# Kernel optimization log

Measured on AMD Instinct MI355X. Metric: run time of the kernel, lower is better.

## Reference

```python
import jax, jax.numpy as jnp
import numpy as np

NUM_EXPERTS = 8
TOP_K = 2
HIDDEN = 1024
INTER = 3584
B, S = 1, 2048


def setup_inputs() -> dict:
    key = jax.random.key(0)
    k0, k1, k2, k3, k4 = jax.random.split(key, 5)
    scale = 0.02
    return {
        "hidden_states": jax.random.normal(k0, (B, S, HIDDEN), dtype=jnp.float32),
        "gate_w": jax.random.normal(k1, (NUM_EXPERTS, HIDDEN), dtype=jnp.float32) * scale,
        "w1": jax.random.normal(k2, (NUM_EXPERTS, INTER, HIDDEN), dtype=jnp.float32) * scale,
        "w2": jax.random.normal(k3, (NUM_EXPERTS, HIDDEN, INTER), dtype=jnp.float32) * scale,
        "w3": jax.random.normal(k4, (NUM_EXPERTS, INTER, HIDDEN), dtype=jnp.float32) * scale,
    }


def reference(hidden_states, gate_w, w1, w2, w3):
    b, s, h = hidden_states.shape
    x = hidden_states.reshape(-1, h)  # [T, H]
    T = x.shape[0]

    # Router: softmax in float32, take top-k, renormalize (normalize_routing_weights=1)
    router_logits = x @ gate_w.T  # [T, E]
    routing_probs = jax.nn.softmax(router_logits.astype(jnp.float32), axis=-1)
    top_w, top_i = jax.lax.top_k(routing_probs, TOP_K)  # [T, K]
    top_w = top_w / jnp.sum(top_w, axis=-1, keepdims=True)
    top_w = top_w.astype(x.dtype)

    # Dense per-token gate matrix [T, E]: weight if expert selected, else 0.
    rows = jnp.arange(T)[:, None]
    gates = jnp.zeros((T, NUM_EXPERTS), dtype=x.dtype).at[rows, top_i].set(top_w)

    # Equivalent to gather-MLP-scatter: y = sum_e gate[:,e] * SwiGLU_e(x)
    out = jnp.zeros((T, h), dtype=x.dtype)
    for e in range(NUM_EXPERTS):
        hid = jax.nn.silu(x @ w1[e].T) * (x @ w3[e].T)  # [T, F]
        out = out + (hid @ w2[e].T) * gates[:, e:e + 1]
    return out.reshape(b, s, h)
```

## Files before the change

### kernel.cpp

```cpp
#include <hip/hip_runtime.h>
#include <hip/hip_bf16.h>
#include <stdint.h>

#define T_TOKENS 2048
#define HID_DIM 1024
#define INTER 3584
#define NEXP 8
#define PTILES 40

typedef float f32x4 __attribute__((ext_vector_type(4)));
typedef short short8 __attribute__((ext_vector_type(8)));
typedef unsigned short ushort8 __attribute__((ext_vector_type(8)));

#define AS1 __attribute__((address_space(1)))
#define AS3 __attribute__((address_space(3)))

__device__ __forceinline__ void gload_lds16(const void* g, void* l) {
    __builtin_amdgcn_global_load_lds((AS1 void*)g, (AS3 void*)l, 16, 0, 0);
}

__device__ __forceinline__ f32x4 mfma16(short8 a, short8 b, f32x4 c) {
    return __builtin_amdgcn_mfma_f32_16x16x32_bf16(a, b, c, 0, 0, 0);
}

__device__ __forceinline__ unsigned short f2bf(float f) {
    union { __hip_bfloat16 h; unsigned short u; } cv;
    cv.h = __float2bfloat16(f);
    return cv.u;
}

__device__ __forceinline__ ushort8 cvt8(float4 v0, float4 v1) {
    ushort8 u;
    u[0] = f2bf(v0.x); u[1] = f2bf(v0.y); u[2] = f2bf(v0.z); u[3] = f2bf(v0.w);
    u[4] = f2bf(v1.x); u[5] = f2bf(v1.y); u[6] = f2bf(v1.z); u[7] = f2bf(v1.w);
    return u;
}

__global__ __launch_bounds__(256) void pack_w_k(const float* __restrict__ w1, const float* __restrict__ w2,
                                                const float* __restrict__ w3,
                                                unsigned short* __restrict__ w1p,
                                                unsigned short* __restrict__ w3p,
                                                unsigned short* __restrict__ w2p) {
    int which = blockIdx.z;
    int e = blockIdx.y;
    const float* src;
    unsigned short* dst;
    int NT, KT, K;
    if (which == 0) { src = w1; dst = w1p; NT = 56; KT = 16; K = HID_DIM; }
    else if (which == 1) { src = w3; dst = w3p; NT = 56; KT = 16; K = HID_DIM; }
    else { src = w2; dst = w2p; NT = 16; KT = 56; K = INTER; }
    int nt = blockIdx.x % NT;
    int kt = blockIdx.x / NT;

    int col = threadIdx.x & 63;
    int kq = threadIdx.x >> 6;
    const float* s = src + ((size_t)(e * (NT * 64) + nt * 64 + col)) * K + kt * 64 + kq * 16;
    float4 v0 = *reinterpret_cast<const float4*>(s);
    float4 v1 = *reinterpret_cast<const float4*>(s + 4);
    float4 v2 = *reinterpret_cast<const float4*>(s + 8);
    float4 v3 = *reinterpret_cast<const float4*>(s + 12);
    unsigned short* d = dst + ((size_t)(e * NT + nt) * KT + kt) * 4096;
    *reinterpret_cast<ushort8*>(d + ((kq * 2 + 0) * 64 + col) * 8) = cvt8(v0, v1);
    *reinterpret_cast<ushort8*>(d + ((kq * 2 + 1) * 64 + col) * 8) = cvt8(v2, v3);
}

__global__ void router_k(const float* __restrict__ x, const float* __restrict__ gw,
                         int* __restrict__ topk_e, float* __restrict__ topk_w,
                         int* __restrict__ ctl) {
    int lane = threadIdx.x & 63;
    int wid = threadIdx.x >> 6;
    int t = blockIdx.x * 4 + wid;
    const float* xr = x + (size_t)t * HID_DIM;

    float acc[NEXP];
#pragma unroll
    for (int e = 0; e < NEXP; ++e) acc[e] = 0.f;

#pragma unroll
    for (int j = 0; j < 4; ++j) {
        int c = j * 256 + lane * 4;
        float4 v = *reinterpret_cast<const float4*>(xr + c);
#pragma unroll
        for (int e = 0; e < NEXP; ++e) {
            float4 g = *reinterpret_cast<const float4*>(gw + e * HID_DIM + c);
            acc[e] += v.x * g.x + v.y * g.y + v.z * g.z + v.w * g.w;
        }
    }
#pragma unroll
    for (int off = 32; off > 0; off >>= 1)
#pragma unroll
        for (int e = 0; e < NEXP; ++e) acc[e] += __shfl_xor(acc[e], off, 64);

    if (lane == 0) {
        int e0 = 0;
#pragma unroll
        for (int e = 1; e < NEXP; ++e) if (acc[e] > acc[e0]) e0 = e;
        int e1 = -1;
        float b1 = 0.f;
#pragma unroll
        for (int e = 0; e < NEXP; ++e) {
            if (e == e0) continue;
            if (e1 < 0 || acc[e] > b1) { e1 = e; b1 = acc[e]; }
        }
        float p1 = __expf(b1 - acc[e0]);
        float s = 1.f + p1;
        topk_e[2 * t] = e0; topk_e[2 * t + 1] = e1;
        topk_w[2 * t] = 1.f / s; topk_w[2 * t + 1] = p1 / s;
        atomicAdd(&ctl[e0], 1);
        atomicAdd(&ctl[e1], 1);
    }
}

__global__ void prefix_k(int* __restrict__ ctl) {
    if (threadIdx.x == 0) {
        int r = 0;
        for (int e = 0; e < NEXP; ++e) {
            ctl[32 + e] = r;
            r += (ctl[e] + 127) & ~127;
            ctl[16 + e] = 0;
        }
    }
}

__global__ void scatter_k(const int* __restrict__ topk_e, const float* __restrict__ topk_w,
                          int* __restrict__ ctl, int* __restrict__ perm_token,
                          float* __restrict__ perm_gate) {
    int t = blockIdx.x * 256 + threadIdx.x;
    if (t >= T_TOKENS) return;
#pragma unroll
    for (int k = 0; k < 2; ++k) {
        int e = topk_e[2 * t + k];
        int p = ctl[32 + e] + atomicAdd(&ctl[16 + e], 1);
        perm_token[p] = t;
        perm_gate[p] = topk_w[2 * t + k];
    }
}

__global__ __launch_bounds__(256) void pack_x_k(const float* __restrict__ x,
                                                const int* __restrict__ perm_token,
                                                unsigned short* __restrict__ xgp) {
    int ptile = blockIdx.x;
    int kt = blockIdx.y;
    int row = threadIdx.x & 127;
    int kh = threadIdx.x >> 7;
    int tok = perm_token[ptile * 128 + row];
    const float* s = x + (size_t)tok * HID_DIM + kt * 64 + kh * 32;
    unsigned short* d = xgp + (size_t)ptile * 131072 + (size_t)kt * 8192;
#pragma unroll
    for (int kb2 = 0; kb2 < 4; ++kb2) {
        int kb = kh * 4 + kb2;
        float4 v0 = *reinterpret_cast<const float4*>(s + kb2 * 8);
        float4 v1 = *reinterpret_cast<const float4*>(s + kb2 * 8 + 4);
        *reinterpret_cast<ushort8*>(d + (kb * 128 + row) * 8) = cvt8(v0, v1);
    }
}

__global__ __launch_bounds__(256) void gemm1_k(
    const unsigned short* __restrict__ xgp,
    const unsigned short* __restrict__ w1p, const unsigned short* __restrict__ w3p,
    const int* __restrict__ ctl, unsigned short* __restrict__ hidp) {
    int e = blockIdx.z;
    int cnt = ctl[e];
    int tm = blockIdx.x;
    if (tm * 128 >= cnt) return;
    int off = ctl[32 + e];
    int nt = blockIdx.y;
    int ptile = (off >> 7) + tm;

    __shared__ __attribute__((aligned(16))) unsigned short A_l[8192];
    __shared__ __attribute__((aligned(16))) unsigned short B1_l[4096];
    __shared__ __attribute__((aligned(16))) unsigned short B3_l[4096];

    int tid = threadIdx.x;
    int lane = tid & 63;
    int wid = tid >> 6;
    int wr = wid >> 1, wc = wid & 1;
    int q = lane >> 4, rr = lane & 15;

    const unsigned short* asrc = xgp + (size_t)ptile * 131072;
    const unsigned short* b1s = w1p + (size_t)(e * 56 + nt) * 65536;
    const unsigned short* b3s = w3p + (size_t)(e * 56 + nt) * 65536;

    f32x4 acc1[4][2], acc3[4][2];
#pragma unroll
    for (int i = 0; i < 4; ++i)
#pragma unroll
        for (int j = 0; j < 2; ++j) { acc1[i][j] = 0.f; acc3[i][j] = 0.f; }

    for (int kt = 0; kt < 16; ++kt) {
        const unsigned short* as = asrc + (size_t)kt * 8192;
        const unsigned short* b1 = b1s + (size_t)kt * 4096;
        const unsigned short* b3 = b3s + (size_t)kt * 4096;
#pragma unroll
        for (int c = 0; c < 4; ++c)
            gload_lds16(as + (c * 256 + tid) * 8, A_l + (c * 256 + tid) * 8);
#pragma unroll
        for (int c = 0; c < 2; ++c) {
            gload_lds16(b1 + (c * 256 + tid) * 8, B1_l + (c * 256 + tid) * 8);
            gload_lds16(b3 + (c * 256 + tid) * 8, B3_l + (c * 256 + tid) * 8);
        }
        __syncthreads();
#pragma unroll
        for (int kk = 0; kk < 2; ++kk) {
            short8 a[4], b1v[2], b3v[2];
            const unsigned short* abase = A_l + (size_t)((kk * 4 + q) * 128 + wr * 64 + rr) * 8;
#pragma unroll
            for (int i = 0; i < 4; ++i) a[i] = *reinterpret_cast<const short8*>(abase + i * 16 * 8);
            const unsigned short* b1base = B1_l + (size_t)((kk * 4 + q) * 64 + wc * 32 + rr) * 8;
            const unsigned short* b3base = B3_l + (size_t)((kk * 4 + q) * 64 + wc * 32 + rr) * 8;
#pragma unroll
            for (int j = 0; j < 2; ++j) {
                b1v[j] = *reinterpret_cast<const short8*>(b1base + j * 16 * 8);
                b3v[j] = *reinterpret_cast<const short8*>(b3base + j * 16 * 8);
            }
#pragma unroll
            for (int i = 0; i < 4; ++i)
#pragma unroll
                for (int j = 0; j < 2; ++j) {
                    acc1[i][j] = mfma16(a[i], b1v[j], acc1[i][j]);
                    acc3[i][j] = mfma16(a[i], b3v[j], acc3[i][j]);
                }
        }
        __syncthreads();
    }

    int rbase = wr * 64 + q * 4;
    int colb = wc * 32 + rr;
    unsigned short* hb = hidp + (size_t)(ptile * 56 + nt) * 8192;
#pragma unroll
    for (int i = 0; i < 4; ++i) {
#pragma unroll
        for (int r = 0; r < 4; ++r) {
            int lrow = rbase + i * 16 + r;
            if (tm * 128 + lrow < cnt) {
#pragma unroll
                for (int j = 0; j < 2; ++j) {
                    int col = colb + j * 16;
                    float g = acc1[i][j][r];
                    float u = acc3[i][j][r];
                    float h = (g / (1.f + __expf(-g))) * u;
                    hb[((col >> 3) * 128 + lrow) * 8 + (col & 7)] = f2bf(h);
                }
            }
        }
    }
}

__global__ __launch_bounds__(256) void gemm2_k(
    const unsigned short* __restrict__ hidp, const unsigned short* __restrict__ w2p,
    const int* __restrict__ ctl, const int* __restrict__ perm_token,
    const float* __restrict__ perm_gate, float* __restrict__ out) {
    int e = blockIdx.z;
    int cnt = ctl[e];
    int tm = blockIdx.x;
    if (tm * 128 >= cnt) return;
    int off = ctl[32 + e];
    int ptile = (off >> 7) + tm;

    __shared__ __attribute__((aligned(16))) unsigned short A_l[8192];
    __shared__ __attribute__((aligned(16))) unsigned short B_l[8192];

    int tid = threadIdx.x;
    int lane = tid & 63;
    int wid = tid >> 6;
    int wr = wid >> 1, wc = wid & 1;
    int q = lane >> 4, rr = lane & 15;

    const unsigned short* asrc = hidp + (size_t)(ptile * 56) * 8192;
    const unsigned short* bs0 = w2p + (size_t)(e * 16 + 2 * blockIdx.y) * 229376;
    const unsigned short* bs1 = bs0 + 229376;

    f32x4 acc[4][4];
#pragma unroll
    for (int i = 0; i < 4; ++i)
#pragma unroll
        for (int j = 0; j < 4; ++j) acc[i][j] = 0.f;

    for (int kt = 0; kt < 56; ++kt) {
        const unsigned short* as = asrc + (size_t)kt * 8192;
        const unsigned short* b0 = bs0 + (size_t)kt * 4096;
        const unsigned short* b1 = bs1 + (size_t)kt * 4096;
#pragma unroll
        for (int c = 0; c < 4; ++c)
            gload_lds16(as + (c * 256 + tid) * 8, A_l + (c * 256 + tid) * 8);
#pragma unroll
        for (int c = 0; c < 2; ++c) {
            gload_lds16(b0 + (c * 256 + tid) * 8, B_l + (c * 256 + tid) * 8);
            gload_lds16(b1 + (c * 256 + tid) * 8, B_l + 4096 + (c * 256 + tid) * 8);
        }
        __syncthreads();
#pragma unroll
        for (int kk = 0; kk < 2; ++kk) {
            short8 a[4], b[4];
            const unsigned short* abase = A_l + (size_t)((kk * 4 + q) * 128 + wr * 64 + rr) * 8;
            const unsigned short* bbase = B_l + (size_t)(wc * 4096) + (size_t)((kk * 4 + q) * 64 + rr) * 8;
#pragma unroll
            for (int i = 0; i < 4; ++i) a[i] = *reinterpret_cast<const short8*>(abase + i * 16 * 8);
#pragma unroll
            for (int j = 0; j < 4; ++j) b[j] = *reinterpret_cast<const short8*>(bbase + j * 16 * 8);
#pragma unroll
            for (int i = 0; i < 4; ++i)
#pragma unroll
                for (int j = 0; j < 4; ++j) acc[i][j] = mfma16(a[i], b[j], acc[i][j]);
        }
        __syncthreads();
    }

    int rb = wr * 64 + q * 4;
    int hb = blockIdx.y * 128 + wc * 64 + rr;
#pragma unroll
    for (int i = 0; i < 4; ++i) {
#pragma unroll
        for (int r = 0; r < 4; ++r) {
            int lrow = rb + i * 16 + r;
            int grow = tm * 128 + lrow;
            if (grow < cnt) {
                int p = off + grow;
                int tok = perm_token[p];
                float gate = perm_gate[p];
#pragma unroll
                for (int j = 0; j < 4; ++j)
                    atomicAdd(&out[(size_t)tok * HID_DIM + hb + j * 16], acc[i][j][r] * gate);
            }
        }
    }
}

extern "C" void kernel_launch(void* const* d_in, const int* in_sizes, int n_in,
                              void* d_out, int out_size, void* d_ws, size_t ws_size,
                              hipStream_t stream) {
    const float* x  = (const float*)d_in[0];
    const float* gw = (const float*)d_in[1];
    const float* w1 = (const float*)d_in[2];
    const float* w2 = (const float*)d_in[3];
    const float* w3 = (const float*)d_in[4];
    float* out = (float*)d_out;

    char* ws = (char*)d_ws;
    int*   ctl        = (int*)ws;
    int*   topk_e     = (int*)(ws + 4096);
    float* topk_w     = (float*)(ws + 20480);
    int*   perm_token = (int*)(ws + 36864);
    float* perm_gate  = (float*)(ws + 57344);
    unsigned short* xgp  = (unsigned short*)(ws + (1ull << 20));
    unsigned short* hidp = (unsigned short*)(ws + 12582912);
    unsigned short* w1p  = (unsigned short*)(ws + 52428800);
    unsigned short* w3p  = (unsigned short*)(ws + 111149056);
    unsigned short* w2p  = (unsigned short*)(ws + 169869312);

    hipMemsetAsync(ctl, 0, 256, stream);
    hipMemsetAsync(perm_token, 0, PTILES * 128 * sizeof(int), stream);
    hipMemsetAsync(out, 0, (size_t)out_size * sizeof(float), stream);

    pack_w_k<<<dim3(896, NEXP, 3), 256, 0, stream>>>(w1, w2, w3, w1p, w3p, w2p);
    router_k<<<dim3(T_TOKENS / 4), 256, 0, stream>>>(x, gw, topk_e, topk_w, ctl);
    prefix_k<<<dim3(1), 64, 0, stream>>>(ctl);
    scatter_k<<<dim3(T_TOKENS / 256), 256, 0, stream>>>(topk_e, topk_w, ctl, perm_token, perm_gate);
    pack_x_k<<<dim3(PTILES, 16), 256, 0, stream>>>(x, perm_token, xgp);
    gemm1_k<<<dim3(PTILES, INTER / 64, NEXP), 256, 0, stream>>>(xgp, w1p, w3p, ctl, hidp);
    gemm2_k<<<dim3(PTILES, HID_DIM / 128, NEXP), 256, 0, stream>>>(hidp, w2p, ctl, perm_token, perm_gate, out);
}
```

Measured before the change: 421.8 us.

## Drop weight pre-pack; stream fp32 weights once per expert tile in GEMMs

Removes the separate pack_w_k pass that converted all expert weights to bf16 in a workspace, which cost a full read of the fp32 weights plus a bf16 write and re-read. The GEMM kernels now load fp32 weight slices directly, convert them to bf16 in LDS with register prefetch of the next k-step, and loop over all token tiles of an expert inside one block so each weight slice is read once. gemm2 also splits K in two with atomics. A operands are read straight from global without LDS staging, which may raise load latency and cost bandwidth.

New measurement: 459.6 us. 9.0% more time.

```diff
diff --git a/kernel.cpp b/kernel.cpp
--- a/kernel.cpp
+++ b/kernel.cpp
@@ -12,13 +12,6 @@
 typedef short short8 __attribute__((ext_vector_type(8)));
 typedef unsigned short ushort8 __attribute__((ext_vector_type(8)));
 
-#define AS1 __attribute__((address_space(1)))
-#define AS3 __attribute__((address_space(3)))
-
-__device__ __forceinline__ void gload_lds16(const void* g, void* l) {
-    __builtin_amdgcn_global_load_lds((AS1 void*)g, (AS3 void*)l, 16, 0, 0);
-}
-
 __device__ __forceinline__ f32x4 mfma16(short8 a, short8 b, f32x4 c) {
     return __builtin_amdgcn_mfma_f32_16x16x32_bf16(a, b, c, 0, 0, 0);
 }
@@ -36,32 +29,10 @@
     return u;
 }
 
-__global__ __launch_bounds__(256) void pack_w_k(const float* __restrict__ w1, const float* __restrict__ w2,
-                                                const float* __restrict__ w3,
-                                                unsigned short* __restrict__ w1p,
-                                                unsigned short* __restrict__ w3p,
-                                                unsigned short* __restrict__ w2p) {
-    int which = blockIdx.z;
-    int e = blockIdx.y;
-    const float* src;
-    unsigned short* dst;
-    int NT, KT, K;
-    if (which == 0) { src = w1; dst = w1p; NT = 56; KT = 16; K = HID_DIM; }
-    else if (which == 1) { src = w3; dst = w3p; NT = 56; KT = 16; K = HID_DIM; }
-    else { src = w2; dst = w2p; NT = 16; KT = 56; K = INTER; }
-    int nt = blockIdx.x % NT;
-    int kt = blockIdx.x / NT;
-
-    int col = threadIdx.x & 63;
-    int kq = threadIdx.x >> 6;
-    const float* s = src + ((size_t)(e * (NT * 64) + nt * 64 + col)) * K + kt * 64 + kq * 16;
-    float4 v0 = *reinterpret_cast<const float4*>(s);
-    float4 v1 = *reinterpret_cast<const float4*>(s + 4);
-    float4 v2 = *reinterpret_cast<const float4*>(s + 8);
-    float4 v3 = *reinterpret_cast<const float4*>(s + 12);
-    unsigned short* d = dst + ((size_t)(e * NT + nt) * KT + kt) * 4096;
-    *reinterpret_cast<ushort8*>(d + ((kq * 2 + 0) * 64 + col) * 8) = cvt8(v0, v1);
-    *reinterpret_cast<ushort8*>(d + ((kq * 2 + 1) * 64 + col) * 8) = cvt8(v2, v3);
+__device__ __forceinline__ ushort4 cvt4(float4 v) {
+    ushort4 u;
+    u.x = f2bf(v.x); u.y = f2bf(v.y); u.z = f2bf(v.z); u.w = f2bf(v.w);
+    return u;
 }
 
 __global__ void router_k(const float* __restrict__ x, const float* __restrict__ gw,
@@ -155,172 +126,187 @@
     }
 }
 
-__global__ __launch_bounds__(256) void gemm1_k(
+__global__ __launch_bounds__(512) void gemm1_k(
     const unsigned short* __restrict__ xgp,
-    const unsigned short* __restrict__ w1p, const unsigned short* __restrict__ w3p,
+    const float* __restrict__ w1, const float* __restrict__ w3,
     const int* __restrict__ ctl, unsigned short* __restrict__ hidp) {
-    int e = blockIdx.z;
+    int e = blockIdx.x & 7;
+    int nt = blockIdx.x >> 3;
     int cnt = ctl[e];
-    int tm = blockIdx.x;
-    if (tm * 128 >= cnt) return;
-    int off = ctl[32 + e];
-    int nt = blockIdx.y;
-    int ptile = (off >> 7) + tm;
-
-    __shared__ __attribute__((aligned(16))) unsigned short A_l[8192];
-    __shared__ __attribute__((aligned(16))) unsigned short B1_l[4096];
-    __shared__ __attribute__((aligned(16))) unsigned short B3_l[4096];
+    if (cnt == 0) return;
+    int ntm = (cnt + 127) >> 7;
+    int pt0 = ctl[32 + e] >> 7;
+
+    __shared__ __attribute__((aligned(16))) unsigned short B_l[8 * 66 * 8];
 
     int tid = threadIdx.x;
     int lane = tid & 63;
-    int wid = tid >> 6;
-    int wr = wid >> 1, wc = wid & 1;
+    int w = tid >> 6;
     int q = lane >> 4, rr = lane & 15;
 
-    const unsigned short* asrc = xgp + (size_t)ptile * 131072;
-    const unsigned short* b1s = w1p + (size_t)(e * 56 + nt) * 65536;
-    const unsigned short* b3s = w3p + (size_t)(e * 56 + nt) * 65536;
-
-    f32x4 acc1[4][2], acc3[4][2];
-#pragma unroll
-    for (int i = 0; i < 4; ++i)
-#pragma unroll
-        for (int j = 0; j < 2; ++j) { acc1[i][j] = 0.f; acc3[i][j] = 0.f; }
-
-    for (int kt = 0; kt < 16; ++kt) {
-        const unsigned short* as = asrc + (size_t)kt * 8192;
-        const unsigned short* b1 = b1s + (size_t)kt * 4096;
-        const unsigned short* b3 = b3s + (size_t)kt * 4096;
-#pragma unroll
-        for (int c = 0; c < 4; ++c)
-            gload_lds16(as + (c * 256 + tid) * 8, A_l + (c * 256 + tid) * 8);
-#pragma unroll
-        for (int c = 0; c < 2; ++c) {
-            gload_lds16(b1 + (c * 256 + tid) * 8, B1_l + (c * 256 + tid) * 8);
-            gload_lds16(b3 + (c * 256 + tid) * 8, B3_l + (c * 256 + tid) * 8);
-        }
-        __syncthreads();
-#pragma unroll
-        for (int kk = 0; kk < 2; ++kk) {
-            short8 a[4], b1v[2], b3v[2];
-            const unsigned short* abase = A_l + (size_t)((kk * 4 + q) * 128 + wr * 64 + rr) * 8;
-#pragma unroll
-            for (int i = 0; i < 4; ++i) a[i] = *reinterpret_cast<const short8*>(abase + i * 16 * 8);
-            const unsigned short* b1base = B1_l + (size_t)((kk * 4 + q) * 64 + wc * 32 + rr) * 8;
-            const unsigned short* b3base = B3_l + (size_t)((kk * 4 + q) * 64 + wc * 32 + rr) * 8;
-#pragma unroll
-            for (int j = 0; j < 2; ++j) {
-                b1v[j] = *reinterpret_cast<const short8*>(b1base + j * 16 * 8);
-                b3v[j] = *reinterpret_cast<const short8*>(b3base + j * 16 * 8);
-            }
-#pragma unroll
-            for (int i = 0; i < 4; ++i)
+    int brow = tid >> 3;
+    int ko = (tid & 7) * 8;
+    const float* wsrc = (brow & 32) ? w3 : w1;
+    const float* bsrc = wsrc + ((size_t)e * INTER + nt * 32 + (brow & 31)) * HID_DIM + ko;
+    int bo = ((tid & 7) * 66 + brow) * 8;
+
+    for (int base = 0; base < ntm; base += 4) {
+        const unsigned short* at[4];
+#pragma unroll
+        for (int tt = 0; tt < 4; ++tt) {
+            int idx = base + tt;
+            at[tt] = xgp + (size_t)(pt0 + (idx < ntm ? idx : 0)) * 131072;
+        }
+        f32x4 acc1[4][2], acc3[4][2];
+#pragma unroll
+        for (int tt = 0; tt < 4; ++tt)
+#pragma unroll
+            for (int j = 0; j < 2; ++j) { acc1[tt][j] = 0.f; acc3[tt][j] = 0.f; }
+
+        float4 f0 = *reinterpret_cast<const float4*>(bsrc);
+        float4 f1 = *reinterpret_cast<const float4*>(bsrc + 4);
+        for (int kt = 0; kt < 16; ++kt) {
+            *reinterpret_cast<ushort8*>(B_l + bo) = cvt8(f0, f1);
+            __syncthreads();
+            if (kt < 15) {
+                f0 = *reinterpret_cast<const float4*>(bsrc + (kt + 1) * 64);
+                f1 = *reinterpret_cast<const float4*>(bsrc + (kt + 1) * 64 + 4);
+            }
+#pragma unroll
+            for (int kk = 0; kk < 2; ++kk) {
+                int ar = ((kk * 4 + q) * 128 + w * 16 + rr) * 8;
+                short8 a[4];
+#pragma unroll
+                for (int tt = 0; tt < 4; ++tt)
+                    a[tt] = *reinterpret_cast<const short8*>(at[tt] + (size_t)kt * 8192 + ar);
+                const unsigned short* bb = B_l + ((kk * 4 + q) * 66 + rr) * 8;
+                short8 b1v[2], b3v[2];
+                b1v[0] = *reinterpret_cast<const short8*>(bb);
+                b1v[1] = *reinterpret_cast<const short8*>(bb + 128);
+                b3v[0] = *reinterpret_cast<const short8*>(bb + 256);
+                b3v[1] = *reinterpret_cast<const short8*>(bb + 384);
+#pragma unroll
+                for (int tt = 0; tt < 4; ++tt)
+#pragma unroll
+                    for (int j = 0; j < 2; ++j) {
+                        acc1[tt][j] = mfma16(a[tt], b1v[j], acc1[tt][j]);
+                        acc3[tt][j] = mfma16(a[tt], b3v[j], acc3[tt][j]);
+                    }
+            }
+            __syncthreads();
+        }
+
+        int lrow = w * 16 + q * 4;
+        int tile56 = nt >> 1;
+        int colbase = (nt & 1) * 32;
+#pragma unroll
+        for (int tt = 0; tt < 4; ++tt) {
+            if (base + tt < ntm) {
+                size_t hb = (size_t)((pt0 + base + tt) * 56 + tile56) * 8192;
+                int rowoff = (base + tt) * 128 + lrow;
 #pragma unroll
                 for (int j = 0; j < 2; ++j) {
-                    acc1[i][j] = mfma16(a[i], b1v[j], acc1[i][j]);
-                    acc3[i][j] = mfma16(a[i], b3v[j], acc3[i][j]);
+                    int hcol = colbase + j * 16 + rr;
+                    int kb = hcol >> 3, w8 = hcol & 7;
+#pragma unroll
+                    for (int ri = 0; ri < 4; ++ri) {
+                        if (rowoff + ri < cnt) {
+                            float g = acc1[tt][j][ri];
+                            float u = acc3[tt][j][ri];
+                            float h = (g / (1.f + __expf(-g))) * u;
+                            hidp[hb + (kb * 128 + lrow + ri) * 8 + w8] = f2bf(h);
+                        }
+                    }
                 }
-        }
-        __syncthreads();
-    }
-
-    int rbase = wr * 64 + q * 4;
-    int colb = wc * 32 + rr;
-    unsigned short* hb = hidp + (size_t)(ptile * 56 + nt) * 8192;
-#pragma unroll
-    for (int i = 0; i < 4; ++i) {
-#pragma unroll
-        for (int r = 0; r < 4; ++r) {
-            int lrow = rbase + i * 16 + r;
-            if (tm * 128 + lrow < cnt) {
-#pragma unroll
-                for (int j = 0; j < 2; ++j) {
-                    int col = colb + j * 16;
-                    float g = acc1[i][j][r];
-                    float u = acc3[i][j][r];
-                    float h = (g / (1.f + __expf(-g))) * u;
-                    hb[((col >> 3) * 128 + lrow) * 8 + (col & 7)] = f2bf(h);
-                }
-            }
-        }
-    }
-}
-
-__global__ __launch_bounds__(256) void gemm2_k(
-    const unsigned short* __restrict__ hidp, const unsigned short* __restrict__ w2p,
+            }
+        }
+    }
+}
+
+__global__ __launch_bounds__(512) void gemm2_k(
+    const unsigned short* __restrict__ hidp, const float* __restrict__ w2,
     const int* __restrict__ ctl, const int* __restrict__ perm_token,
     const float* __restrict__ perm_gate, float* __restrict__ out) {
-    int e = blockIdx.z;
+    int e = blockIdx.x & 7;
+    int nt = (blockIdx.x >> 3) & 31;
+    int ks = blockIdx.x >> 8;
     int cnt = ctl[e];
-    int tm = blockIdx.x;
-    if (tm * 128 >= cnt) return;
+    if (cnt == 0) return;
+    int ntm = (cnt + 127) >> 7;
     int off = ctl[32 + e];
-    int ptile = (off >> 7) + tm;
-
-    __shared__ __attribute__((aligned(16))) unsigned short A_l[8192];
-    __shared__ __attribute__((aligned(16))) unsigned short B_l[8192];
+    int pt0 = off >> 7;
+
+    __shared__ __attribute__((aligned(16))) unsigned short B_l[8 * 34 * 8];
 
     int tid = threadIdx.x;
     int lane = tid & 63;
-    int wid = tid >> 6;
-    int wr = wid >> 1, wc = wid & 1;
+    int w = tid >> 6;
     int q = lane >> 4, rr = lane & 15;
 
-    const unsigned short* asrc = hidp + (size_t)(ptile * 56) * 8192;
-    const unsigned short* bs0 = w2p + (size_t)(e * 16 + 2 * blockIdx.y) * 229376;
-    const unsigned short* bs1 = bs0 + 229376;
-
-    f32x4 acc[4][4];
-#pragma unroll
-    for (int i = 0; i < 4; ++i)
-#pragma unroll
-        for (int j = 0; j < 4; ++j) acc[i][j] = 0.f;
-
-    for (int kt = 0; kt < 56; ++kt) {
-        const unsigned short* as = asrc + (size_t)kt * 8192;
-        const unsigned short* b0 = bs0 + (size_t)kt * 4096;
-        const unsigned short* b1 = bs1 + (size_t)kt * 4096;
-#pragma unroll
-        for (int c = 0; c < 4; ++c)
-            gload_lds16(as + (c * 256 + tid) * 8, A_l + (c * 256 + tid) * 8);
-#pragma unroll
-        for (int c = 0; c < 2; ++c) {
-            gload_lds16(b0 + (c * 256 + tid) * 8, B_l + (c * 256 + tid) * 8);
-            gload_lds16(b1 + (c * 256 + tid) * 8, B_l + 4096 + (c * 256 + tid) * 8);
-        }
-        __syncthreads();
-#pragma unroll
-        for (int kk = 0; kk < 2; ++kk) {
-            short8 a[4], b[4];
-            const unsigned short* abase = A_l + (size_t)((kk * 4 + q) * 128 + wr * 64 + rr) * 8;
-            const unsigned short* bbase = B_l + (size_t)(wc * 4096) + (size_t)((kk * 4 + q) * 64 + rr) * 8;
-#pragma unroll
-            for (int i = 0; i < 4; ++i) a[i] = *reinterpret_cast<const short8*>(abase + i * 16 * 8);
-#pragma unroll
-            for (int j = 0; j < 4; ++j) b[j] = *reinterpret_cast<const short8*>(bbase + j * 16 * 8);
-#pragma unroll
-            for (int i = 0; i < 4; ++i)
-#pragma unroll
-                for (int j = 0; j < 4; ++j) acc[i][j] = mfma16(a[i], b[j], acc[i][j]);
-        }
-        __syncthreads();
-    }
-
-    int rb = wr * 64 + q * 4;
-    int hb = blockIdx.y * 128 + wc * 64 + rr;
-#pragma unroll
-    for (int i = 0; i < 4; ++i) {
-#pragma unroll
-        for (int r = 0; r < 4; ++r) {
-            int lrow = rb + i * 16 + r;
-            int grow = tm * 128 + lrow;
-            if (grow < cnt) {
-                int p = off + grow;
-                int tok = perm_token[p];
-                float gate = perm_gate[p];
-#pragma unroll
-                for (int j = 0; j < 4; ++j)
-                    atomicAdd(&out[(size_t)tok * HID_DIM + hb + j * 16], acc[i][j][r] * gate);
+    int brow = tid >> 4;
+    int ko = (tid & 15) * 4;
+    const float* bsrc = w2 + ((size_t)e * HID_DIM + nt * 32 + brow) * INTER + (size_t)ks * 28 * 64 + ko;
+    int bo = ((ko >> 3) * 34 + brow) * 8 + (ko & 7);
+
+    int kt0 = ks * 28;
+    for (int base = 0; base < ntm; base += 4) {
+        const unsigned short* at[4];
+#pragma unroll
+        for (int tt = 0; tt < 4; ++tt) {
+            int idx = base + tt;
+            at[tt] = hidp + (size_t)(pt0 + (idx < ntm ? idx : 0)) * 56 * 8192;
+        }
+        f32x4 acc[4][2];
+#pragma unroll
+        for (int tt = 0; tt < 4; ++tt)
+#pragma unroll
+            for (int j = 0; j < 2; ++j) acc[tt][j] = 0.f;
+
+        float4 f0 = *reinterpret_cast<const float4*>(bsrc);
+        for (int t = 0; t < 28; ++t) {
+            int kt = kt0 + t;
+            *reinterpret_cast<ushort4*>(B_l + bo) = cvt4(f0);
+            __syncthreads();
+            if (t < 27) f0 = *reinterpret_cast<const float4*>(bsrc + (t + 1) * 64);
+#pragma unroll
+            for (int kk = 0; kk < 2; ++kk) {
+                int ar = ((kk * 4 + q) * 128 + w * 16 + rr) * 8;
+                short8 a[4];
+#pragma unroll
+                for (int tt = 0; tt < 4; ++tt)
+                    a[tt] = *reinterpret_cast<const short8*>(at[tt] + (size_t)kt * 8192 + ar);
+                const unsigned short* bb = B_l + ((kk * 4 + q) * 34 + rr) * 8;
+                short8 b[2];
+                b[0] = *reinterpret_cast<const short8*>(bb);
+                b[1] = *reinterpret_cast<const short8*>(bb + 128);
+#pragma unroll
+                for (int tt = 0; tt < 4; ++tt)
+#pragma unroll
+                    for (int j = 0; j < 2; ++j)
+                        acc[tt][j] = mfma16(a[tt], b[j], acc[tt][j]);
+            }
+            __syncthreads();
+        }
+
+        int lrow = w * 16 + q * 4;
+#pragma unroll
+        for (int tt = 0; tt < 4; ++tt) {
+            if (base + tt < ntm) {
+                int rowoff = (base + tt) * 128 + lrow;
+#pragma unroll
+                for (int ri = 0; ri < 4; ++ri) {
+                    int grow = rowoff + ri;
+                    if (grow < cnt) {
+                        int p = off + grow;
+                        int tok = perm_token[p];
+                        float gate = perm_gate[p];
+#pragma unroll
+                        for (int j = 0; j < 2; ++j) {
+                            int col = nt * 32 + j * 16 + rr;
+                            atomicAdd(&out[(size_t)tok * HID_DIM + col], acc[tt][j][ri] * gate);
+                        }
+                    }
+                }
             }
         }
     }
@@ -344,19 +330,15 @@
     float* perm_gate  = (float*)(ws + 57344);
     unsigned short* xgp  = (unsigned short*)(ws + (1ull << 20));
     unsigned short* hidp = (unsigned short*)(ws + 12582912);
-    unsigned short* w1p  = (unsigned short*)(ws + 52428800);
-    unsigned short* w3p  = (unsigned short*)(ws + 111149056);
-    unsigned short* w2p  = (unsigned short*)(ws + 169869312);
-
-    hipMemsetAsync(ctl, 0, 256, stream);
+
+    hipMemsetAsync(ctl, 0, 512, stream);
     hipMemsetAsync(perm_token, 0, PTILES * 128 * sizeof(int), stream);
     hipMemsetAsync(out, 0, (size_t)out_size * sizeof(float), stream);
 
-    pack_w_k<<<dim3(896, NEXP, 3), 256, 0, stream>>>(w1, w2, w3, w1p, w3p, w2p);
     router_k<<<dim3(T_TOKENS / 4), 256, 0, stream>>>(x, gw, topk_e, topk_w, ctl);
     prefix_k<<<dim3(1), 64, 0, stream>>>(ctl);
     scatter_k<<<dim3(T_TOKENS / 256), 256, 0, stream>>>(topk_e, topk_w, ctl, perm_token, perm_gate);
     pack_x_k<<<dim3(PTILES, 16), 256, 0, stream>>>(x, perm_token, xgp);
-    gemm1_k<<<dim3(PTILES, INTER / 64, NEXP), 256, 0, stream>>>(xgp, w1p, w3p, ctl, hidp);
-    gemm2_k<<<dim3(PTILES, HID_DIM / 128, NEXP), 256, 0, stream>>>(hidp, w2p, ctl, perm_token, perm_gate, out);
-}
+    gemm1_k<<<dim3(896), 512, 0, stream>>>(xgp, w1, w3, ctl, hidp);
+    gemm2_k<<<dim3(512), 512, 0, stream>>>(hidp, w2, ctl, perm_token, perm_gate, out);
+}
```
